# Kernel tuning notes

Measured on AMD Instinct MI355X. Metric: run time of the kernel, lower is better.

## Reference

```python
import jax, jax.numpy as jnp
import numpy as np

N = 100000   # nodes per type
E = 300000   # edges per relation
IN = 128     # input feature dim
H = 4        # heads
C = 32       # hidden_channels per head
D = H * C    # concat output dim
R = 8        # relations
# node type order: 0=transaction, 1=account, 2=device, 3=ip, 4=email
# relations: by, rev_by, uses, rev_uses, from_ip, rev_from_ip, with_email, rev_with_email
REL = [(0, 1), (1, 0), (0, 2), (2, 0), (0, 3), (3, 0), (0, 4), (4, 0)]


def setup_inputs() -> dict:
    key = jax.random.key(0)
    ks = jax.random.split(key, 18)
    s = 0.05
    return {
        "x_transaction": jax.random.normal(ks[0], (N, IN), jnp.float32),
        "x_account": jax.random.normal(ks[1], (N, IN), jnp.float32),
        "x_device": jax.random.normal(ks[2], (N, IN), jnp.float32),
        "x_ip": jax.random.normal(ks[3], (N, IN), jnp.float32),
        "x_email": jax.random.normal(ks[4], (N, IN), jnp.float32),
        "edges": jax.random.randint(ks[5], (R, 2, E), 0, N, dtype=jnp.int32),
        "Ws1": jax.random.normal(ks[6], (R, IN, D), jnp.float32) * s,
        "Wd1": jax.random.normal(ks[7], (R, IN, D), jnp.float32) * s,
        "as1": jax.random.normal(ks[8], (R, H, C), jnp.float32) * s,
        "ad1": jax.random.normal(ks[9], (R, H, C), jnp.float32) * s,
        "b1": jnp.zeros((R, D), jnp.float32),
        "Ws2": jax.random.normal(ks[10], (R, D, D), jnp.float32) * s,
        "Wd2": jax.random.normal(ks[11], (R, D, D), jnp.float32) * s,
        "as2": jax.random.normal(ks[12], (R, H, C), jnp.float32) * s,
        "ad2": jax.random.normal(ks[13], (R, H, C), jnp.float32) * s,
        "b2": jnp.zeros((R, D), jnp.float32),
    }


def _gat_layer(xs, edges, Ws, Wd, a_s, a_d, b):
    """One HeteroConv layer of per-relation GATConv with sum-aggregation over relations."""
    outs = [jnp.zeros((x.shape[0], D), x.dtype) for x in xs]
    for r, (si, di) in enumerate(REL):
        Nd = xs[di].shape[0]
        hs = (xs[si] @ Ws[r]).reshape(-1, H, C)   # [Ns,H,C]
        hd = (xs[di] @ Wd[r]).reshape(-1, H, C)   # [Nd,H,C]
        es = jnp.einsum('nhc,hc->nh', hs, a_s[r])  # per-src logit term
        ed = jnp.einsum('nhc,hc->nh', hd, a_d[r])  # per-dst logit term
        src, dst = edges[r, 0], edges[r, 1]
        logit = jax.nn.leaky_relu(es[src] + ed[dst], 0.2)          # [E,H]
        m = jax.ops.segment_max(logit, dst, num_segments=Nd)       # segment-softmax (stable)
        m = jnp.where(jnp.isfinite(m), m, 0.0)
        p = jnp.exp(logit - m[dst])
        denom = jax.ops.segment_sum(p, dst, num_segments=Nd)
        alpha = p / (denom[dst] + 1e-16)                           # [E,H]
        agg = jax.ops.segment_sum(hs[src] * alpha[:, :, None], dst, num_segments=Nd)
        outs[di] = outs[di] + agg.reshape(Nd, D) + b[r]
    return outs


def reference(x_transaction, x_account, x_device, x_ip, x_email, edges,
              Ws1, Wd1, as1, ad1, b1, Ws2, Wd2, as2, ad2, b2):
    xs = [x_transaction, x_account, x_device, x_ip, x_email]
    xs = [jax.nn.elu(h) for h in _gat_layer(xs, edges, Ws1, Wd1, as1, ad1, b1)]
    xs = [jax.nn.elu(h) for h in _gat_layer(xs, edges, Ws2, Wd2, as2, ad2, b2)]
    return jnp.stack(xs)  # [5, N, D] in node-type order tx/acc/dev/ip/email
```

## Files before the change

### kernel.cpp

```cpp
#include <hip/hip_runtime.h>

#define NRELS 8
typedef __attribute__((ext_vector_type(8))) short s16x8;
typedef __attribute__((ext_vector_type(4))) float f32x4;
typedef unsigned short u16;
typedef unsigned int u32;

__device__ __forceinline__ u16 f2bf(float v) {
    unsigned u = __float_as_uint(v);
    u += 0x7FFFu + ((u >> 16) & 1u);
    return (u16)(u >> 16);
}
__device__ __forceinline__ float bf2f(u16 h) {
    return __uint_as_float(((unsigned)h) << 16);
}
__device__ __forceinline__ float eluf(float x) { return x > 0.f ? x : __expf(x) - 1.f; }

__global__ void prep_weights(const float* __restrict__ Ws1, const float* __restrict__ Wd1,
                             const float* __restrict__ as1, const float* __restrict__ ad1,
                             const float* __restrict__ b1,
                             const float* __restrict__ Ws2, const float* __restrict__ Wd2,
                             const float* __restrict__ as2, const float* __restrict__ ad2,
                             const float* __restrict__ b2,
                             u16* __restrict__ Wfrag, float* __restrict__ bperm,
                             float* __restrict__ b0sum) {
    const int bid = blockIdx.x;
    if (bid >= 16) {
        const int layer = bid - 16;
        const float* bb = layer ? b2 : b1;
        if (threadIdx.x < 128) {
            int p = threadIdx.x;
            int oc = ((p & 7) << 4) | (p >> 3);
            b0sum[layer * 128 + p] = bb[1 * 128 + oc] + bb[3 * 128 + oc]
                                   + bb[5 * 128 + oc] + bb[7 * 128 + oc];
        }
        return;
    }
    const int layer = bid >> 3, r = bid & 7, r1 = r ^ 1;
    const float* Ws  = (layer ? Ws2 : Ws1) + (size_t)r  * 16384;
    const float* asp = (layer ? as2 : as1) + r  * 128;
    const float* Wdr = (layer ? Wd2 : Wd1) + (size_t)r1 * 16384;
    const float* adr = (layer ? ad2 : ad1) + r1 * 128;
    const float* bb  = (layer ? b2  : b1 ) + r  * 128;
    u16* wf = Wfrag + (size_t)bid * 18432;
    for (int f = threadIdx.x; f < 18432; f += blockDim.x) {
        int be   = f & 7;
        int lane = (f >> 3) & 63;
        int kc   = (f >> 9) & 3;
        int ct   = f >> 11;
        int k    = kc * 32 + (lane >> 4) * 8 + be;
        int krow = layer ? (((k & 7) << 4) | (k >> 3)) : k;
        int c    = lane & 15;
        float val;
        if (ct < 8) {
            val = Ws[(size_t)krow * 128 + ct * 16 + c];
        } else if (c < 4) {
            float s = 0.f;
            #pragma unroll
            for (int cc = 0; cc < 32; ++cc) s += Ws[(size_t)krow * 128 + c * 32 + cc] * asp[c * 32 + cc];
            val = s;
        } else if (c < 8) {
            int h = c - 4;
            float s = 0.f;
            #pragma unroll
            for (int cc = 0; cc < 32; ++cc) s += Wdr[(size_t)krow * 128 + h * 32 + cc] * adr[h * 32 + cc];
            val = s;
        } else {
            val = 0.f;
        }
        wf[f] = f2bf(val);
    }
    if (threadIdx.x < 128) {
        int p = threadIdx.x;
        bperm[bid * 128 + p] = bb[((p & 7) << 4) | (p >> 3)];
    }
}

template<int FP32IN>
__global__ __launch_bounds__(256) void gemm_mfma(
        const float* __restrict__ x0, const float* __restrict__ x1,
        const float* __restrict__ x2, const float* __restrict__ x3,
        const float* __restrict__ x4,
        const u16* __restrict__ Xbf, const u16* __restrict__ WfragL,
        u16* __restrict__ Hs8, float* __restrict__ es8, float* __restrict__ ed8, int N) {
    __shared__ u16 wlds[18432];
    const int y = blockIdx.y;
    int rel0, nph, stype;
    if (y < 2) { rel0 = y * 4;         nph = 2; stype = 0; }
    else       { rel0 = 2 * (y - 2) + 1; nph = 1; stype = y - 1; }

    const int tid = threadIdx.x;
    const int wv = tid >> 6, l = tid & 63;
    const int lr = l & 15, lk = l >> 4;
    const int r0 = blockIdx.x * 128 + wv * 32;

    s16x8 af[2][4];
    if (FP32IN) {
        const float* Xf = stype == 0 ? x0 : stype == 1 ? x1 : stype == 2 ? x2
                        : stype == 3 ? x3 : x4;
        #pragma unroll
        for (int rt = 0; rt < 2; ++rt) {
            int row = r0 + rt * 16 + lr;
            if (row > N - 1) row = N - 1;
            const float* xp = Xf + (size_t)row * 128 + lk * 8;
            #pragma unroll
            for (int q = 0; q < 4; ++q) {
                float4 v0 = *(const float4*)(xp + q * 32);
                float4 v1 = *(const float4*)(xp + q * 32 + 4);
                s16x8 f;
                f[0] = (short)f2bf(v0.x); f[1] = (short)f2bf(v0.y);
                f[2] = (short)f2bf(v0.z); f[3] = (short)f2bf(v0.w);
                f[4] = (short)f2bf(v1.x); f[5] = (short)f2bf(v1.y);
                f[6] = (short)f2bf(v1.z); f[7] = (short)f2bf(v1.w);
                af[rt][q] = f;
            }
        }
    } else {
        const u16* X = Xbf + (size_t)stype * N * 128;
        #pragma unroll
        for (int rt = 0; rt < 2; ++rt) {
            int row = r0 + rt * 16 + lr;
            if (row > N - 1) row = N - 1;
            const s16x8* xp = (const s16x8*)(X + (size_t)row * 128 + lk * 8);
            af[rt][0] = xp[0]; af[rt][1] = xp[4]; af[rt][2] = xp[8]; af[rt][3] = xp[12];
        }
    }

    for (int ph = 0; ph < nph; ++ph) {
        const int r = rel0 + ph * 2;
        const u16* Wf = WfragL + (size_t)r * 18432;
        __syncthreads();
        for (int i = tid; i < 2304; i += 256)
            ((s16x8*)wlds)[i] = ((const s16x8*)Wf)[i];
        __syncthreads();

        f32x4 acc[2][9] = {};
        #pragma unroll
        for (int ct = 0; ct < 9; ++ct) {
            s16x8 bf0 = ((s16x8*)wlds)[(ct * 4 + 0) * 64 + l];
            s16x8 bf1 = ((s16x8*)wlds)[(ct * 4 + 1) * 64 + l];
            s16x8 bf2 = ((s16x8*)wlds)[(ct * 4 + 2) * 64 + l];
            s16x8 bf3 = ((s16x8*)wlds)[(ct * 4 + 3) * 64 + l];
            #pragma unroll
            for (int rt = 0; rt < 2; ++rt) {
                acc[rt][ct] = __builtin_amdgcn_mfma_f32_16x16x32_bf16(af[rt][0], bf0, acc[rt][ct], 0, 0, 0);
                acc[rt][ct] = __builtin_amdgcn_mfma_f32_16x16x32_bf16(af[rt][1], bf1, acc[rt][ct], 0, 0, 0);
                acc[rt][ct] = __builtin_amdgcn_mfma_f32_16x16x32_bf16(af[rt][2], bf2, acc[rt][ct], 0, 0, 0);
                acc[rt][ct] = __builtin_amdgcn_mfma_f32_16x16x32_bf16(af[rt][3], bf3, acc[rt][ct], 0, 0, 0);
            }
        }

        u16*   Hs = Hs8 + (size_t)r * N * 128;
        float* es = es8 + (size_t)r * N * 4;
        float* ed = ed8 + (size_t)(r ^ 1) * N * 4;
        #pragma unroll
        for (int rt = 0; rt < 2; ++rt) {
            #pragma unroll
            for (int j = 0; j < 4; ++j) {
                int row = r0 + rt * 16 + lk * 4 + j;
                if (row < N) {
                    union { u16 u[8]; uint4 q; } pk;
                    #pragma unroll
                    for (int ct = 0; ct < 8; ++ct) pk.u[ct] = f2bf(acc[rt][ct][j]);
                    *(uint4*)(Hs + (size_t)row * 128 + lr * 8) = pk.q;
                    float evv = acc[rt][8][j];
                    if (lr < 4)      es[(size_t)row * 4 + lr]     = evv;
                    else if (lr < 8) ed[(size_t)row * 4 + lr - 4] = evv;
                }
            }
        }
    }
}

__global__ void hist_kernel(const int* __restrict__ edges, int* __restrict__ counts,
                            int E, int N) {
    int r = blockIdx.x & 7;
    int e = (blockIdx.x >> 3) * 256 + threadIdx.x;
    if (e >= E) return;
    int d = edges[(size_t)r * 2 * E + E + e];
    atomicAdd(&counts[r * N + d], 1);
}

__global__ __launch_bounds__(256) void scan_block_k(const int* __restrict__ in,
                                                    int* __restrict__ outv,
                                                    int* __restrict__ bsum, int M) {
    __shared__ int sh[256];
    int t = threadIdx.x;
    int base = blockIdx.x * 2048 + t * 8;
    int vals[8];
    int tot = 0;
    #pragma unroll
    for (int j = 0; j < 8; ++j) {
        int v = (base + j < M) ? in[base + j] : 0;
        vals[j] = tot; tot += v;
    }
    sh[t] = tot;
    __syncthreads();
    for (int ofs = 1; ofs < 256; ofs <<= 1) {
        int y = 0;
        if (t >= ofs) y = sh[t - ofs];
        __syncthreads();
        if (t >= ofs) sh[t] += y;
        __syncthreads();
    }
    int ex = (t == 0) ? 0 : sh[t - 1];
    #pragma unroll
    for (int j = 0; j < 8; ++j)
        if (base + j < M) outv[base + j] = ex + vals[j];
    if (t == 255) bsum[blockIdx.x] = sh[255];
}

__global__ __launch_bounds__(1024) void scan_tops_k(const int* __restrict__ bsum,
                                                    int* __restrict__ bpref, int nb) {
    __shared__ int sh[1024];
    int t = threadIdx.x;
    int v = (t < nb) ? bsum[t] : 0;
    sh[t] = v;
    __syncthreads();
    for (int ofs = 1; ofs < 1024; ofs <<= 1) {
        int y = 0;
        if (t >= ofs) y = sh[t - ofs];
        __syncthreads();
        if (t >= ofs) sh[t] += y;
        __syncthreads();
    }
    if (t < nb) bpref[t] = sh[t] - v;
}

__global__ void scan_add_k(int* __restrict__ outv, int* __restrict__ pos,
                           const int* __restrict__ bpref, int M) {
    int g = blockIdx.x * blockDim.x + threadIdx.x;
    if (g < M) {
        int v = outv[g] + bpref[g >> 11];
        outv[g] = v;
        pos[g] = v;
    }
}

__global__ void build_csr_k(const int* __restrict__ edges, int* __restrict__ pos,
                            int* __restrict__ srcs, int E, int N) {
    int r = blockIdx.x & 7;
    int e = (blockIdx.x >> 3) * 256 + threadIdx.x;
    if (e >= E) return;
    const int* b = edges + (size_t)r * 2 * E;
    int s = b[e], d = b[E + e];
    int idx = atomicAdd(&pos[r * N + d], 1);
    srcs[idx] = s;
}

__global__ __launch_bounds__(256) void pnorm_k(
        const int* __restrict__ srcsG, const int* __restrict__ offs,
        const int* __restrict__ counts, const float* __restrict__ es8,
        const float* __restrict__ ed8, float* __restrict__ pcsr, int N) {
    const int r = blockIdx.y;
    const int* OFF = offs + (size_t)r * N;
    const int* CNT = counts + (size_t)r * N;
    const float* ES = es8 + (size_t)r * N * 4;
    const float* ED = ed8 + (size_t)r * N * 4;
    int g = blockIdx.x * 256 + threadIdx.x;
    if (g >= N * 4) return;
    const int d = g >> 2, h = g & 3;
    const int o0 = OFF[d], dg = CNT[d];
    if (dg == 0) return;
    const float edv = ED[(size_t)d * 4 + h];
    float lc[8];
    float mx = -INFINITY;
    #pragma unroll
    for (int i = 0; i < 8; ++i) {
        if (i < dg) {
            int s = srcsG[o0 + i];
            float lv = ES[(size_t)s * 4 + h] + edv;
            lv = lv > 0.f ? lv : 0.2f * lv;
            lc[i] = lv;
            mx = fmaxf(mx, lv);
        }
    }
    for (int i = 8; i < dg; ++i) {
        int s = srcsG[o0 + i];
        float lv = ES[(size_t)s * 4 + h] + edv;
        lv = lv > 0.f ? lv : 0.2f * lv;
        mx = fmaxf(mx, lv);
    }
    float den = 0.f;
    #pragma unroll
    for (int i = 0; i < 8; ++i) {
        if (i < dg) { lc[i] = __expf(lc[i] - mx); den += lc[i]; }
    }
    for (int i = 8; i < dg; ++i) {
        int s = srcsG[o0 + i];
        float lv = ES[(size_t)s * 4 + h] + edv;
        lv = lv > 0.f ? lv : 0.2f * lv;
        den += __expf(lv - mx);
    }
    const float inv = 1.f / (den + 1e-16f);
    #pragma unroll
    for (int i = 0; i < 8; ++i) {
        if (i < dg) pcsr[(size_t)(o0 + i) * 4 + h] = lc[i] * inv;
    }
    for (int i = 8; i < dg; ++i) {
        int s = srcsG[o0 + i];
        float lv = ES[(size_t)s * 4 + h] + edv;
        lv = lv > 0.f ? lv : 0.2f * lv;
        pcsr[(size_t)(o0 + i) * 4 + h] = __expf(lv - mx) * inv;
    }
}

__device__ __forceinline__ void acc_rel(float a[8], const int* __restrict__ srcsG,
        const float* __restrict__ pcsr, const int* __restrict__ OFF,
        const int* __restrict__ CNT, const u16* __restrict__ HS,
        int ds, bool act, int ln) {
    const int o0 = OFF[ds];
    const int dg = act ? CNT[ds] : 0;
    if (dg == 0) return;
    #pragma unroll
    for (int i = 0; i < 4; ++i) {
        int idx = o0 + (i < dg ? i : dg - 1);
        int s = srcsG[idx];
        float4 p4 = *(const float4*)(pcsr + (size_t)idx * 4);
        uint4 hv  = *(const uint4*)(HS + (size_t)s * 128 + 8 * ln);
        if (i >= dg) { p4.x = 0.f; p4.y = 0.f; p4.z = 0.f; p4.w = 0.f; }
        a[0] += p4.x * bf2f((u16)(hv.x & 0xFFFF)); a[1] += p4.x * bf2f((u16)(hv.x >> 16));
        a[2] += p4.y * bf2f((u16)(hv.y & 0xFFFF)); a[3] += p4.y * bf2f((u16)(hv.y >> 16));
        a[4] += p4.z * bf2f((u16)(hv.z & 0xFFFF)); a[5] += p4.z * bf2f((u16)(hv.z >> 16));
        a[6] += p4.w * bf2f((u16)(hv.w & 0xFFFF)); a[7] += p4.w * bf2f((u16)(hv.w >> 16));
    }
    #pragma unroll
    for (int i = 4; i < 8; ++i) {
        if (i < dg) {
            int idx = o0 + i;
            int s = srcsG[idx];
            float4 p4 = *(const float4*)(pcsr + (size_t)idx * 4);
            uint4 hv  = *(const uint4*)(HS + (size_t)s * 128 + 8 * ln);
            a[0] += p4.x * bf2f((u16)(hv.x & 0xFFFF)); a[1] += p4.x * bf2f((u16)(hv.x >> 16));
            a[2] += p4.y * bf2f((u16)(hv.y & 0xFFFF)); a[3] += p4.y * bf2f((u16)(hv.y >> 16));
            a[4] += p4.z * bf2f((u16)(hv.z & 0xFFFF)); a[5] += p4.z * bf2f((u16)(hv.z >> 16));
            a[6] += p4.w * bf2f((u16)(hv.w & 0xFFFF)); a[7] += p4.w * bf2f((u16)(hv.w >> 16));
        }
    }
    for (int i = 8; i < dg; ++i) {
        int idx = o0 + i;
        int s = srcsG[idx];
        float4 p4 = *(const float4*)(pcsr + (size_t)idx * 4);
        uint4 hv  = *(const uint4*)(HS + (size_t)s * 128 + 8 * ln);
        a[0] += p4.x * bf2f((u16)(hv.x & 0xFFFF)); a[1] += p4.x * bf2f((u16)(hv.x >> 16));
        a[2] += p4.y * bf2f((u16)(hv.y & 0xFFFF)); a[3] += p4.y * bf2f((u16)(hv.y >> 16));
        a[4] += p4.z * bf2f((u16)(hv.z & 0xFFFF)); a[5] += p4.z * bf2f((u16)(hv.z >> 16));
        a[6] += p4.w * bf2f((u16)(hv.w & 0xFFFF)); a[7] += p4.w * bf2f((u16)(hv.w >> 16));
    }
}

template<int OUT_MODE>
__global__ __launch_bounds__(256) void gat_all(
        const int* __restrict__ srcsG, const float* __restrict__ pcsr,
        const int* __restrict__ offs, const int* __restrict__ counts,
        const u16* __restrict__ Hs8, const float* __restrict__ bpermL,
        const float* __restrict__ b0sumL, void* __restrict__ outBase, int N) {
    const int y   = blockIdx.y;
    const int tid = threadIdx.x;
    const int ln  = tid & 15;
    const int d   = (blockIdx.x * 256 + tid) >> 4;
    const bool act = (d < N);
    const int ds = act ? d : 0;

    float a[8] = {};
    const float* bb;
    size_t slice;
    if (y == 0) {
        #pragma unroll
        for (int rr = 0; rr < 4; ++rr) {
            const int rel = 2 * rr + 1;
            acc_rel(a, srcsG, pcsr, offs + (size_t)rel * N, counts + (size_t)rel * N,
                    Hs8 + (size_t)rel * N * 128, ds, act, ln);
        }
        bb = b0sumL;
        slice = 0;
    } else {
        const int rel = 2 * (y - 1);
        acc_rel(a, srcsG, pcsr, offs + (size_t)rel * N, counts + (size_t)rel * N,
                Hs8 + (size_t)rel * N * 128, ds, act, ln);
        bb = bpermL + (size_t)rel * 128;
        slice = (size_t)y * N * 128;
    }
    if (!act) return;

    float4 b0 = *(const float4*)(bb + 8 * ln);
    float4 b1 = *(const float4*)(bb + 8 * ln + 4);
    a[0] += b0.x; a[1] += b0.y; a[2] += b0.z; a[3] += b0.w;
    a[4] += b1.x; a[5] += b1.y; a[6] += b1.z; a[7] += b1.w;

    if (OUT_MODE == 0) {
        u16* OP = (u16*)outBase + slice;
        union { u16 u[8]; uint4 q; } pk;
        #pragma unroll
        for (int j = 0; j < 8; ++j) pk.u[j] = f2bf(eluf(a[j]));
        *(uint4*)(OP + (size_t)d * 128 + 8 * ln) = pk.q;
    } else {
        float* OP = (float*)outBase + slice;
        float* o = OP + (size_t)d * 128;
        #pragma unroll
        for (int j = 0; j < 8; ++j)
            o[(j << 4) | ln] = eluf(a[j]);
    }
}

extern "C" void kernel_launch(void* const* d_in, const int* in_sizes, int n_in,
                              void* d_out, int out_size, void* d_ws, size_t ws_size,
                              hipStream_t stream) {
    const int N = in_sizes[0] / 128;
    const int E = in_sizes[5] / (2 * NRELS);

    const float* xs0[5] = { (const float*)d_in[0], (const float*)d_in[1],
                            (const float*)d_in[2], (const float*)d_in[3],
                            (const float*)d_in[4] };
    const int*   edges = (const int*)d_in[5];
    const float* Ws1 = (const float*)d_in[6];
    const float* Wd1 = (const float*)d_in[7];
    const float* as1 = (const float*)d_in[8];
    const float* ad1 = (const float*)d_in[9];
    const float* b1  = (const float*)d_in[10];
    const float* Ws2 = (const float*)d_in[11];
    const float* Wd2 = (const float*)d_in[12];
    const float* as2 = (const float*)d_in[13];
    const float* ad2 = (const float*)d_in[14];
    const float* b2  = (const float*)d_in[15];
    float* out = (float*)d_out;

    char* wp = (char*)d_ws;
    u16*   Xbf   = (u16*)wp;   wp += (size_t)5 * N * 128 * 2;
    u16*   Hs8   = (u16*)wp;   wp += (size_t)8 * N * 128 * 2;
    float* es8   = (float*)wp; wp += (size_t)8 * N * 4 * 4;
    float* ed8   = (float*)wp; wp += (size_t)8 * N * 4 * 4;
    float* pcsr  = (float*)wp; wp += (size_t)NRELS * E * 4 * 4;
    int* counts  = (int*)wp;   wp += (size_t)NRELS * N * 4;
    int* offs    = (int*)wp;   wp += (size_t)NRELS * N * 4;
    int* pos     = (int*)wp;   wp += (size_t)NRELS * N * 4;
    int* srcs    = (int*)wp;   wp += (size_t)NRELS * E * 4;
    u16* Wfrag   = (u16*)wp;   wp += (size_t)16 * 18432 * 2;
    float* bperm = (float*)wp; wp += (size_t)16 * 128 * 4;
    float* b0sum = (float*)wp; wp += (size_t)2 * 128 * 4;
    int* bsum    = (int*)wp;   wp += 1024 * 4;
    int* bpref   = (int*)wp;   wp += 1024 * 4;
    const size_t ws_used = (size_t)(wp - (char*)d_ws);
    if (ws_used > ws_size) return;

    const int M = NRELS * N;
    hipMemsetAsync(counts, 0, (size_t)M * 4, stream);

    prep_weights<<<dim3(18), 256, 0, stream>>>(Ws1, Wd1, as1, ad1, b1,
                                               Ws2, Wd2, as2, ad2, b2,
                                               Wfrag, bperm, b0sum);

    const int nb = (M + 2047) / 2048;
    const int eblocks = 8 * ((E + 255) / 256);
    hist_kernel<<<dim3(eblocks), 256, 0, stream>>>(edges, counts, E, N);
    scan_block_k<<<dim3(nb), 256, 0, stream>>>(counts, offs, bsum, M);
    scan_tops_k<<<dim3(1), 1024, 0, stream>>>(bsum, bpref, nb);
    scan_add_k<<<dim3((M + 255) / 256), 256, 0, stream>>>(offs, pos, bpref, M);
    build_csr_k<<<dim3(eblocks), 256, 0, stream>>>(edges, pos, srcs, E, N);

    const int gemmBlocks  = (N + 127) / 128;
    const int gBlocks     = (N + 15) / 16;
    const int pnormBlocks = (N * 4 + 255) / 256;

    for (int layer = 0; layer < 2; ++layer) {
        const u16*   WL = Wfrag + (size_t)layer * 8 * 18432;
        const float* bL = bperm + layer * 8 * 128;

        if (layer == 0)
            gemm_mfma<1><<<dim3(gemmBlocks, 6), 256, 0, stream>>>(
                xs0[0], xs0[1], xs0[2], xs0[3], xs0[4], nullptr, WL, Hs8, es8, ed8, N);
        else
            gemm_mfma<0><<<dim3(gemmBlocks, 6), 256, 0, stream>>>(
                nullptr, nullptr, nullptr, nullptr, nullptr, Xbf, WL, Hs8, es8, ed8, N);

        pnorm_k<<<dim3(pnormBlocks, 8), 256, 0, stream>>>(
            srcs, offs, counts, es8, ed8, pcsr, N);

        if (layer == 0)
            gat_all<0><<<dim3(gBlocks, 5), 256, 0, stream>>>(
                srcs, pcsr, offs, counts, Hs8, bL, b0sum + 0 * 128, Xbf, N);
        else
            gat_all<2><<<dim3(gBlocks, 5), 256, 0, stream>>>(
                srcs, pcsr, offs, counts, Hs8, bL, b0sum + 1 * 128, out, N);
    }
}
```

Before: 922.4 us.

## Merge histogram into weight prep, overlap CSR build with layer-1 GEMM, coalesce output stores

The edge-degree histogram is folded into the weight-prep kernel, and the CSR scatter is interleaved as extra blocks inside the layer-1 GEMM launch, so the scatter's atomic traffic can overlap with MFMA work and two launches go away. The final fp32 output path now stages results through shared memory and writes contiguous float4 rows instead of strided scalar stores. In exchange, the fused GEMM grid is padded with idle blocks, its edge blocks reserve the GEMM's LDS allocation and may lower occupancy, and the output kernel gains a block-wide barrier plus extra shared memory.

```diff
diff --git a/kernel.cpp b/kernel.cpp
--- a/kernel.cpp
+++ b/kernel.cpp
@@ -16,15 +16,26 @@
 }
 __device__ __forceinline__ float eluf(float x) { return x > 0.f ? x : __expf(x) - 1.f; }
 
-__global__ void prep_weights(const float* __restrict__ Ws1, const float* __restrict__ Wd1,
-                             const float* __restrict__ as1, const float* __restrict__ ad1,
-                             const float* __restrict__ b1,
-                             const float* __restrict__ Ws2, const float* __restrict__ Wd2,
-                             const float* __restrict__ as2, const float* __restrict__ ad2,
-                             const float* __restrict__ b2,
-                             u16* __restrict__ Wfrag, float* __restrict__ bperm,
-                             float* __restrict__ b0sum) {
+__global__ void prep_hist(const float* __restrict__ Ws1, const float* __restrict__ Wd1,
+                          const float* __restrict__ as1, const float* __restrict__ ad1,
+                          const float* __restrict__ b1,
+                          const float* __restrict__ Ws2, const float* __restrict__ Wd2,
+                          const float* __restrict__ as2, const float* __restrict__ ad2,
+                          const float* __restrict__ b2,
+                          u16* __restrict__ Wfrag, float* __restrict__ bperm,
+                          float* __restrict__ b0sum,
+                          const int* __restrict__ edges, int* __restrict__ counts,
+                          int E, int N) {
     const int bid = blockIdx.x;
+    if (bid >= 18) {
+        const int hb = bid - 18;
+        const int r = hb & 7;
+        const int e = (hb >> 3) * 256 + threadIdx.x;
+        if (e >= E) return;
+        int d = edges[(size_t)r * 2 * E + E + e];
+        atomicAdd(&counts[r * N + d], 1);
+        return;
+    }
     if (bid >= 16) {
         const int layer = bid - 16;
         const float* bb = layer ? b2 : b1;
@@ -76,56 +87,11 @@
     }
 }
 
-template<int FP32IN>
-__global__ __launch_bounds__(256) void gemm_mfma(
-        const float* __restrict__ x0, const float* __restrict__ x1,
-        const float* __restrict__ x2, const float* __restrict__ x3,
-        const float* __restrict__ x4,
-        const u16* __restrict__ Xbf, const u16* __restrict__ WfragL,
-        u16* __restrict__ Hs8, float* __restrict__ es8, float* __restrict__ ed8, int N) {
-    __shared__ u16 wlds[18432];
-    const int y = blockIdx.y;
-    int rel0, nph, stype;
-    if (y < 2) { rel0 = y * 4;         nph = 2; stype = 0; }
-    else       { rel0 = 2 * (y - 2) + 1; nph = 1; stype = y - 1; }
-
-    const int tid = threadIdx.x;
-    const int wv = tid >> 6, l = tid & 63;
-    const int lr = l & 15, lk = l >> 4;
-    const int r0 = blockIdx.x * 128 + wv * 32;
-
-    s16x8 af[2][4];
-    if (FP32IN) {
-        const float* Xf = stype == 0 ? x0 : stype == 1 ? x1 : stype == 2 ? x2
-                        : stype == 3 ? x3 : x4;
-        #pragma unroll
-        for (int rt = 0; rt < 2; ++rt) {
-            int row = r0 + rt * 16 + lr;
-            if (row > N - 1) row = N - 1;
-            const float* xp = Xf + (size_t)row * 128 + lk * 8;
-            #pragma unroll
-            for (int q = 0; q < 4; ++q) {
-                float4 v0 = *(const float4*)(xp + q * 32);
-                float4 v1 = *(const float4*)(xp + q * 32 + 4);
-                s16x8 f;
-                f[0] = (short)f2bf(v0.x); f[1] = (short)f2bf(v0.y);
-                f[2] = (short)f2bf(v0.z); f[3] = (short)f2bf(v0.w);
-                f[4] = (short)f2bf(v1.x); f[5] = (short)f2bf(v1.y);
-                f[6] = (short)f2bf(v1.z); f[7] = (short)f2bf(v1.w);
-                af[rt][q] = f;
-            }
-        }
-    } else {
-        const u16* X = Xbf + (size_t)stype * N * 128;
-        #pragma unroll
-        for (int rt = 0; rt < 2; ++rt) {
-            int row = r0 + rt * 16 + lr;
-            if (row > N - 1) row = N - 1;
-            const s16x8* xp = (const s16x8*)(X + (size_t)row * 128 + lk * 8);
-            af[rt][0] = xp[0]; af[rt][1] = xp[4]; af[rt][2] = xp[8]; af[rt][3] = xp[12];
-        }
-    }
-
+__device__ __forceinline__ void gemm_phases(const s16x8 af[2][4], u16* wlds,
+        const u16* __restrict__ WfragL, int rel0, int nph,
+        u16* __restrict__ Hs8, float* __restrict__ es8, float* __restrict__ ed8,
+        int r0, int N, int tid) {
+    const int l = tid & 63, lr = l & 15, lk = l >> 4;
     for (int ph = 0; ph < nph; ++ph) {
         const int r = rel0 + ph * 2;
         const u16* Wf = WfragL + (size_t)r * 18432;
@@ -172,13 +138,91 @@
     }
 }
 
-__global__ void hist_kernel(const int* __restrict__ edges, int* __restrict__ counts,
-                            int E, int N) {
-    int r = blockIdx.x & 7;
-    int e = (blockIdx.x >> 3) * 256 + threadIdx.x;
-    if (e >= E) return;
-    int d = edges[(size_t)r * 2 * E + E + e];
-    atomicAdd(&counts[r * N + d], 1);
+__device__ __forceinline__ void ymap(int y, int& rel0, int& nph, int& stype) {
+    if (y < 2) { rel0 = y * 4;           nph = 2; stype = 0; }
+    else       { rel0 = 2 * (y - 2) + 1; nph = 1; stype = y - 1; }
+}
+
+__global__ __launch_bounds__(256) void gemm1_build(
+        const float* __restrict__ x0, const float* __restrict__ x1,
+        const float* __restrict__ x2, const float* __restrict__ x3,
+        const float* __restrict__ x4,
+        const u16* __restrict__ WfragL,
+        u16* __restrict__ Hs8, float* __restrict__ es8, float* __restrict__ ed8,
+        const int* __restrict__ edges, int* __restrict__ pos, int* __restrict__ srcs,
+        int gemmBlocks, int E, int N) {
+    __shared__ u16 wlds[18432];
+    const int bx = blockIdx.x;
+    const int q = bx / 3, rm = bx % 3;
+    const int tid = threadIdx.x;
+
+    if (rm != 0) {
+        const int bi = bx - q - 1;
+        const int nEB = (E + 255) / 256;
+        if (bi >= 8 * nEB) return;
+        const int rel = bi & 7;
+        const int e = (bi >> 3) * 256 + tid;
+        if (e >= E) return;
+        const int* b = edges + (size_t)rel * 2 * E;
+        int s = b[e], d = b[E + e];
+        int idx = atomicAdd(&pos[rel * N + d], 1);
+        srcs[idx] = s;
+        return;
+    }
+    if (q >= gemmBlocks * 6) return;
+    const int gx = q % gemmBlocks;
+    const int y  = q / gemmBlocks;
+    int rel0, nph, stype;
+    ymap(y, rel0, nph, stype);
+
+    const int l = tid & 63, lr = l & 15, lk = l >> 4;
+    const int wv = tid >> 6;
+    const int r0 = gx * 128 + wv * 32;
+
+    const float* Xf = stype == 0 ? x0 : stype == 1 ? x1 : stype == 2 ? x2
+                    : stype == 3 ? x3 : x4;
+    s16x8 af[2][4];
+    #pragma unroll
+    for (int rt = 0; rt < 2; ++rt) {
+        int row = r0 + rt * 16 + lr;
+        if (row > N - 1) row = N - 1;
+        const float* xp = Xf + (size_t)row * 128 + lk * 8;
+        #pragma unroll
+        for (int qq = 0; qq < 4; ++qq) {
+            float4 v0 = *(const float4*)(xp + qq * 32);
+            float4 v1 = *(const float4*)(xp + qq * 32 + 4);
+            s16x8 f;
+            f[0] = (short)f2bf(v0.x); f[1] = (short)f2bf(v0.y);
+            f[2] = (short)f2bf(v0.z); f[3] = (short)f2bf(v0.w);
+            f[4] = (short)f2bf(v1.x); f[5] = (short)f2bf(v1.y);
+            f[6] = (short)f2bf(v1.z); f[7] = (short)f2bf(v1.w);
+            af[rt][qq] = f;
+        }
+    }
+    gemm_phases(af, wlds, WfragL, rel0, nph, Hs8, es8, ed8, r0, N, tid);
+}
+
+__global__ __launch_bounds__(256) void gemm2_mfma(
+        const u16* __restrict__ Xbf, const u16* __restrict__ WfragL,
+        u16* __restrict__ Hs8, float* __restrict__ es8, float* __restrict__ ed8, int N) {
+    __shared__ u16 wlds[18432];
+    const int tid = threadIdx.x;
+    int rel0, nph, stype;
+    ymap(blockIdx.y, rel0, nph, stype);
+    const int l = tid & 63, lr = l & 15, lk = l >> 4;
+    const int wv = tid >> 6;
+    const int r0 = blockIdx.x * 128 + wv * 32;
+
+    const u16* X = Xbf + (size_t)stype * N * 128;
+    s16x8 af[2][4];
+    #pragma unroll
+    for (int rt = 0; rt < 2; ++rt) {
+        int row = r0 + rt * 16 + lr;
+        if (row > N - 1) row = N - 1;
+        const s16x8* xp = (const s16x8*)(X + (size_t)row * 128 + lk * 8);
+        af[rt][0] = xp[0]; af[rt][1] = xp[4]; af[rt][2] = xp[8]; af[rt][3] = xp[12];
+    }
+    gemm_phases(af, wlds, WfragL, rel0, nph, Hs8, es8, ed8, r0, N, tid);
 }
 
 __global__ __launch_bounds__(256) void scan_block_k(const int* __restrict__ in,
@@ -235,17 +279,6 @@
         outv[g] = v;
         pos[g] = v;
     }
-}
-
-__global__ void build_csr_k(const int* __restrict__ edges, int* __restrict__ pos,
-                            int* __restrict__ srcs, int E, int N) {
-    int r = blockIdx.x & 7;
-    int e = (blockIdx.x >> 3) * 256 + threadIdx.x;
-    if (e >= E) return;
-    const int* b = edges + (size_t)r * 2 * E;
-    int s = b[e], d = b[E + e];
-    int idx = atomicAdd(&pos[r * N + d], 1);
-    srcs[idx] = s;
 }
 
 __global__ __launch_bounds__(256) void pnorm_k(
@@ -355,6 +388,7 @@
         const int* __restrict__ offs, const int* __restrict__ counts,
         const u16* __restrict__ Hs8, const float* __restrict__ bpermL,
         const float* __restrict__ b0sumL, void* __restrict__ outBase, int N) {
+    __shared__ float stg[4][4][128];
     const int y   = blockIdx.y;
     const int tid = threadIdx.x;
     const int ln  = tid & 15;
@@ -381,7 +415,6 @@
         bb = bpermL + (size_t)rel * 128;
         slice = (size_t)y * N * 128;
     }
-    if (!act) return;
 
     float4 b0 = *(const float4*)(bb + 8 * ln);
     float4 b1 = *(const float4*)(bb + 8 * ln + 4);
@@ -389,17 +422,26 @@
     a[4] += b1.x; a[5] += b1.y; a[6] += b1.z; a[7] += b1.w;
 
     if (OUT_MODE == 0) {
-        u16* OP = (u16*)outBase + slice;
-        union { u16 u[8]; uint4 q; } pk;
-        #pragma unroll
-        for (int j = 0; j < 8; ++j) pk.u[j] = f2bf(eluf(a[j]));
-        *(uint4*)(OP + (size_t)d * 128 + 8 * ln) = pk.q;
+        if (act) {
+            u16* OP = (u16*)outBase + slice;
+            union { u16 u[8]; uint4 q; } pk;
+            #pragma unroll
+            for (int j = 0; j < 8; ++j) pk.u[j] = f2bf(eluf(a[j]));
+            *(uint4*)(OP + (size_t)d * 128 + 8 * ln) = pk.q;
+        }
     } else {
-        float* OP = (float*)outBase + slice;
-        float* o = OP + (size_t)d * 128;
-        #pragma unroll
-        for (int j = 0; j < 8; ++j)
-            o[(j << 4) | ln] = eluf(a[j]);
+        const int wv = tid >> 6, gl = (tid >> 4) & 3;
+        if (act) {
+            #pragma unroll
+            for (int j = 0; j < 8; ++j)
+                stg[wv][gl][(j << 4) | ln] = eluf(a[j]);
+        }
+        __syncthreads();
+        if (act) {
+            float* o = (float*)outBase + slice + (size_t)d * 128;
+            *(float4*)(o + 8 * ln)     = *(float4*)&stg[wv][gl][8 * ln];
+            *(float4*)(o + 8 * ln + 4) = *(float4*)&stg[wv][gl][8 * ln + 4];
+        }
     }
 }
 
@@ -446,32 +488,37 @@
     const int M = NRELS * N;
     hipMemsetAsync(counts, 0, (size_t)M * 4, stream);
 
-    prep_weights<<<dim3(18), 256, 0, stream>>>(Ws1, Wd1, as1, ad1, b1,
-                                               Ws2, Wd2, as2, ad2, b2,
-                                               Wfrag, bperm, b0sum);
+    const int nEB = (E + 255) / 256;
+    const int eblocks = 8 * nEB;
+
+    prep_hist<<<dim3(18 + eblocks), 256, 0, stream>>>(
+        Ws1, Wd1, as1, ad1, b1, Ws2, Wd2, as2, ad2, b2,
+        Wfrag, bperm, b0sum, edges, counts, E, N);
 
     const int nb = (M + 2047) / 2048;
-    const int eblocks = 8 * ((E + 255) / 256);
-    hist_kernel<<<dim3(eblocks), 256, 0, stream>>>(edges, counts, E, N);
     scan_block_k<<<dim3(nb), 256, 0, stream>>>(counts, offs, bsum, M);
     scan_tops_k<<<dim3(1), 1024, 0, stream>>>(bsum, bpref, nb);
     scan_add_k<<<dim3((M + 255) / 256), 256, 0, stream>>>(offs, pos, bpref, M);
-    build_csr_k<<<dim3(eblocks), 256, 0, stream>>>(edges, pos, srcs, E, N);
 
     const int gemmBlocks  = (N + 127) / 128;
+    const int G6          = gemmBlocks * 6;
     const int gBlocks     = (N + 15) / 16;
     const int pnormBlocks = (N * 4 + 255) / 256;
+
+    const int K = (G6 > (eblocks + 1) / 2) ? G6 : (eblocks + 1) / 2;
 
     for (int layer = 0; layer < 2; ++layer) {
         const u16*   WL = Wfrag + (size_t)layer * 8 * 18432;
         const float* bL = bperm + layer * 8 * 128;
 
-        if (layer == 0)
-            gemm_mfma<1><<<dim3(gemmBlocks, 6), 256, 0, stream>>>(
-                xs0[0], xs0[1], xs0[2], xs0[3], xs0[4], nullptr, WL, Hs8, es8, ed8, N);
-        else
-            gemm_mfma<0><<<dim3(gemmBlocks, 6), 256, 0, stream>>>(
-                nullptr, nullptr, nullptr, nullptr, nullptr, Xbf, WL, Hs8, es8, ed8, N);
+        if (layer == 0) {
+            gemm1_build<<<dim3(3 * K), 256, 0, stream>>>(
+                xs0[0], xs0[1], xs0[2], xs0[3], xs0[4],
+                WL, Hs8, es8, ed8, edges, pos, srcs, gemmBlocks, E, N);
+        } else {
+            gemm2_mfma<<<dim3(gemmBlocks, 6), 256, 0, stream>>>(
+                Xbf, WL, Hs8, es8, ed8, N);
+        }
 
         pnorm_k<<<dim3(pnormBlocks, 8), 256, 0, stream>>>(
             srcs, offs, counts, es8, ed8, pcsr, N);
```

Result: faster. 860.3 us (-6.7%).
